# Performance work log

Measured on AMD Instinct MI355X. Metric: run time of the kernel, lower is better.

The kernel has to match this reference:

```python
import jax, jax.numpy as jnp
import numpy as np

NUM_HEADS = 16
D_MODEL = 1024
DEPTH = D_MODEL // NUM_HEADS


def rope_sincos(seq_len, depth):
    # standard RoPE: inv_freq over even dims, sin/cos tiled to full depth
    inv_freq = 1.0 / (10000.0 ** (jnp.arange(0, depth, 2, dtype=jnp.float32) / depth))
    ang = jnp.arange(seq_len, dtype=jnp.float32)[:, None] * inv_freq[None, :]  # [S, depth/2]
    sin = jnp.concatenate([jnp.sin(ang), jnp.sin(ang)], axis=-1)  # [S, depth]
    cos = jnp.concatenate([jnp.cos(ang), jnp.cos(ang)], axis=-1)
    return sin, cos


def apply_rope(x, sin, cos):
    # x: [B,H,S,depth]; rotate-half formulation
    half = x.shape[-1] // 2
    x1, x2 = x[..., :half], x[..., half:]
    rot = jnp.concatenate([-x2, x1], axis=-1)
    return x * cos + rot * sin


def setup_inputs() -> dict:
    key = jax.random.key(0)
    ks = jax.random.split(key, 5)
    s = 1.0 / np.sqrt(D_MODEL)
    return {
        "x": jax.random.normal(ks[0], (2, 2048, D_MODEL), dtype=jnp.float32),
        "wq": jax.random.normal(ks[1], (D_MODEL, D_MODEL), dtype=jnp.float32) * s,
        "bq": jnp.zeros((D_MODEL,), jnp.float32),
        "wk": jax.random.normal(ks[2], (D_MODEL, D_MODEL), dtype=jnp.float32) * s,
        "bk": jnp.zeros((D_MODEL,), jnp.float32),
        "wv": jax.random.normal(ks[3], (D_MODEL, D_MODEL), dtype=jnp.float32) * s,
        "bv": jnp.zeros((D_MODEL,), jnp.float32),
        "wo": jax.random.normal(ks[4], (D_MODEL, D_MODEL), dtype=jnp.float32) * s,
        "bo": jnp.zeros((D_MODEL,), jnp.float32),
    }


def reference(x, wq, bq, wk, bk, wv, bv, wo, bo):
    B, S, _ = x.shape

    def split_heads(t):  # [B,S,D] -> [B,H,S,depth]
        return t.reshape(B, S, NUM_HEADS, DEPTH).transpose(0, 2, 1, 3)

    Q = split_heads(x @ wq + bq)
    K = split_heads(x @ wk + bk)
    V = split_heads(x @ wv + bv)

    sin, cos = rope_sincos(S, DEPTH)  # [S, depth], broadcasts over B,H
    Q = apply_rope(Q, sin, cos)
    K = apply_rope(K, sin, cos)

    scores = jnp.einsum("bhqd,bhkd->bhqk", Q, K) / jnp.sqrt(jnp.float32(DEPTH))
    weights = jax.nn.softmax(scores, axis=-1)
    out = jnp.einsum("bhqk,bhkd->bhqd", weights, V)
    out = out.transpose(0, 2, 1, 3).reshape(B, S, D_MODEL)
    return out @ wo + bo
```

## Files before the change

kernel.cpp:

```cpp
#include <hip/hip_runtime.h>

#define DM 1024
#define SEQ 2048
#define NH 16
#define DH 64
#define BATCH 2

typedef _Float16 half_t;
typedef _Float16 half8 __attribute__((ext_vector_type(8)));
typedef _Float16 half4 __attribute__((ext_vector_type(4)));
typedef __fp16 f16x2 __attribute__((ext_vector_type(2)));
typedef unsigned u32x2 __attribute__((ext_vector_type(2)));
typedef unsigned u32x4 __attribute__((ext_vector_type(4)));
typedef float f32x4 __attribute__((ext_vector_type(4)));

__device__ __forceinline__ f32x4 mfma16(half8 a, half8 b, f32x4 c) {
  return __builtin_amdgcn_mfma_f32_16x16x32_f16(a, b, c, 0, 0, 0);
}
__device__ __forceinline__ f32x4 mfma16k16(half4 a, half4 b, f32x4 c) {
  return __builtin_amdgcn_mfma_f32_16x16x16f16(a, b, c, 0, 0, 0);
}

__device__ __forceinline__ void gl2lds16(const half_t* g, half_t* l) {
  __builtin_amdgcn_global_load_lds((const __attribute__((address_space(1))) void*)g,
                                   (__attribute__((address_space(3))) void*)l, 16, 0, 0);
}


__global__ void cvt_x_kernel(const float* __restrict__ x, half_t* __restrict__ xh) {
  int i = (blockIdx.x * 256 + threadIdx.x) * 4;
  float4 v = *(const float4*)(x + i);
  half4 h = { (half_t)v.x, (half_t)v.y, (half_t)v.z, (half_t)v.w };
  *(half4*)(xh + i) = h;
}

__global__ void wtrans_kernel(const float* __restrict__ w0, const float* __restrict__ w1,
                              const float* __restrict__ w2, const float* __restrict__ w3,
                              half_t* __restrict__ o0, half_t* __restrict__ o1,
                              half_t* __restrict__ o2, half_t* __restrict__ o3) {
  __shared__ float tile[32][33];
  const float* w = (blockIdx.z == 0) ? w0 : (blockIdx.z == 1) ? w1 : (blockIdx.z == 2) ? w2 : w3;
  half_t* o = (blockIdx.z == 0) ? o0 : (blockIdx.z == 1) ? o1 : (blockIdx.z == 2) ? o2 : o3;
  int tx = threadIdx.x, ty0 = threadIdx.y;
  int bx = blockIdx.x * 32, by = blockIdx.y * 32;
#pragma unroll
  for (int i = 0; i < 4; i++) {
    int ty = ty0 + i * 8;
    tile[ty][tx] = w[(size_t)(by + ty) * DM + bx + tx];
  }
  __syncthreads();
#pragma unroll
  for (int i = 0; i < 4; i++) {
    int ty = ty0 + i * 8;
    o[(size_t)(bx + ty) * DM + by + tx] = (half_t)tile[tx][ty];
  }
}

__global__ void ropetab_kernel(float* __restrict__ st, float* __restrict__ ct) {
  int idx = blockIdx.x * 256 + threadIdx.x;
  int s = idx >> 5, i = idx & 31;
  float freq = exp2f(-(float)i * (13.287712379549449f / 32.0f));
  float ang = (float)s * freq;
  st[idx] = sinf(ang);
  ct[idx] = cosf(ang);
}


__global__ __launch_bounds__(256)
void qkv_kernel(const half_t* __restrict__ xh,
                const half_t* __restrict__ wtq, const half_t* __restrict__ wtk,
                const half_t* __restrict__ wtv,
                const float* __restrict__ bq, const float* __restrict__ bk,
                const float* __restrict__ bv,
                const float* __restrict__ st, const float* __restrict__ ctab,
                half_t* __restrict__ Qh, half_t* __restrict__ Kh, half_t* __restrict__ Vt) {
  const int tid = threadIdx.x;
  const int wid = tid >> 6, lane = tid & 63;
  const int l16 = lane & 15, quad = lane >> 4;
  const int m0 = blockIdx.y * 128, n0 = blockIdx.x * 128;
  const int g = blockIdx.z;
  const half_t* wt = (g == 0) ? wtq : (g == 1) ? wtk : wtv;
  const float* bias = (g == 0) ? bq : (g == 1) ? bk : bv;
  __shared__ __align__(16) char smem[32768];
  f32x4 acc[4][4] = {};
  const int wrow = (wid >> 1) * 64, wcol = (wid & 1) * 64;

  const int ar0 = tid >> 2,          ab0 = (tid & 3) ^ ((ar0 >> 1) & 3);
  const int ar1 = (tid + 256) >> 2,  ab1 = (tid & 3) ^ ((ar1 >> 1) & 3);
  const int swz = (l16 >> 1) & 3;

  {
    half_t* As = (half_t*)smem;
    half_t* Bs = (half_t*)(smem + 16384);
    gl2lds16(&xh[(size_t)(m0 + ar0) * DM + ab0 * 8], &As[tid * 8]);
    gl2lds16(&xh[(size_t)(m0 + ar1) * DM + ab1 * 8], &As[(tid + 256) * 8]);
    gl2lds16(&wt[(size_t)(n0 + ar0) * DM + ab0 * 8], &Bs[tid * 8]);
    gl2lds16(&wt[(size_t)(n0 + ar1) * DM + ab1 * 8], &Bs[(tid + 256) * 8]);
  }
  __syncthreads();

  int cur = 0;
  for (int k0 = 0; k0 < DM; k0 += 32) {
    if (k0 + 32 < DM) {
      half_t* Asn = (half_t*)(smem + (cur ^ 1) * 8192);
      half_t* Bsn = (half_t*)(smem + 16384 + (cur ^ 1) * 8192);
      const int kn = k0 + 32;
      gl2lds16(&xh[(size_t)(m0 + ar0) * DM + kn + ab0 * 8], &Asn[tid * 8]);
      gl2lds16(&xh[(size_t)(m0 + ar1) * DM + kn + ab1 * 8], &Asn[(tid + 256) * 8]);
      gl2lds16(&wt[(size_t)(n0 + ar0) * DM + kn + ab0 * 8], &Bsn[tid * 8]);
      gl2lds16(&wt[(size_t)(n0 + ar1) * DM + kn + ab1 * 8], &Bsn[(tid + 256) * 8]);
    }
    const half_t* Asc = (const half_t*)(smem + cur * 8192);
    const half_t* Bsc = (const half_t*)(smem + 16384 + cur * 8192);
    half8 a[4], b[4];
#pragma unroll
    for (int rt = 0; rt < 4; rt++)
      a[rt] = *(const half8*)&Asc[((wrow + rt * 16 + l16) * 4 + (quad ^ swz)) * 8];
#pragma unroll
    for (int ct = 0; ct < 4; ct++)
      b[ct] = *(const half8*)&Bsc[((wcol + ct * 16 + l16) * 4 + (quad ^ swz)) * 8];
#pragma unroll
    for (int rt = 0; rt < 4; rt++)
#pragma unroll
      for (int ct = 0; ct < 4; ct++)
        acc[rt][ct] = mfma16(a[rt], b[ct], acc[rt][ct]);
    __syncthreads();
    cur ^= 1;
  }

  const int h = (n0 + wcol) >> 6;
  const float qscale = 0.125f * 1.44269504089f;
  float bv4[4];
#pragma unroll
  for (int ct = 0; ct < 4; ct++) bv4[ct] = bias[n0 + wcol + ct * 16 + l16];

  if (g == 2) {
    half_t* vt = (half_t*)(smem + wid * 8192);
#pragma unroll
    for (int rt = 0; rt < 4; rt++)
#pragma unroll
      for (int ct = 0; ct < 4; ct++) {
        half4 hv;
#pragma unroll
        for (int r = 0; r < 4; r++) hv[r] = (half_t)(acc[rt][ct][r] + bv4[ct]);
        int row = ct * 16 + l16;
        int colu = rt * 2 + (quad >> 1);
        *(half4*)&vt[row * 64 + ((colu ^ (row & 7)) * 8) + (quad & 1) * 4] = hv;
      }
    const int sb = m0 + wrow;
    const int bb = sb >> 11, s0 = sb & 2047;
    half_t* dstv = Vt + (size_t)(bb * NH + h) * DH * SEQ;
#pragma unroll
    for (int i = 0; i < 8; i++) {
      int d = i * 8 + (lane >> 3), c = lane & 7;
      half8 v = *(const half8*)&vt[d * 64 + ((c ^ (d & 7)) * 8)];
      *(half8*)&dstv[(size_t)d * SEQ + s0 + c * 8] = v;
    }
  } else {
    half_t* dst = (g == 0) ? Qh : Kh;
#pragma unroll
    for (int rt = 0; rt < 4; rt++) {
#pragma unroll
      for (int r = 0; r < 4; r++) {
        int m = m0 + wrow + rt * 16 + quad * 4 + r;
        int bb = m >> 11, s = m & 2047;
        float v0 = acc[rt][0][r] + bv4[0];
        float v1 = acc[rt][1][r] + bv4[1];
        float v2 = acc[rt][2][r] + bv4[2];
        float v3 = acc[rt][3][r] + bv4[3];
        float sn0 = st[s * 32 + l16], cs0 = ctab[s * 32 + l16];
        float sn1 = st[s * 32 + 16 + l16], cs1 = ctab[s * 32 + 16 + l16];
        float o0 = v0 * cs0 - v2 * sn0;
        float o1 = v1 * cs1 - v3 * sn1;
        float o2 = v2 * cs0 + v0 * sn0;
        float o3 = v3 * cs1 + v1 * sn1;
        if (g == 0) { o0 *= qscale; o1 *= qscale; o2 *= qscale; o3 *= qscale; }
        size_t base = ((size_t)(bb * NH + h) * SEQ + s) * DH;
        dst[base + l16]      = (half_t)o0;
        dst[base + 16 + l16] = (half_t)o1;
        dst[base + 32 + l16] = (half_t)o2;
        dst[base + 48 + l16] = (half_t)o3;
      }
    }
  }
}


__global__ __launch_bounds__(512)
void attn_kernel(const half_t* __restrict__ Qh, const half_t* __restrict__ Kh,
                 const half_t* __restrict__ Vt, half_t* __restrict__ AO) {
  const int tid = threadIdx.x;
  const int wid = tid >> 6, lane = tid & 63;
  const int l16 = lane & 15, quad = lane >> 4;
  const int lid = blockIdx.x;
  const int bh = lid & 31, qt = lid >> 5;
  const int bb = bh >> 4, h = bh & 15;
  const int q0 = qt * 256 + wid * 32;
  const half_t* Q = Qh + (size_t)bh * SEQ * DH;
  const half_t* K = Kh + (size_t)bh * SEQ * DH;
  const half_t* V = Vt + (size_t)bh * DH * SEQ;
  __shared__ __align__(16) half_t Ks[2][64 * 64];
  __shared__ __align__(16) half_t Vs[2][64 * 64];

  const int r0 = tid >> 3, c0 = (tid & 7) ^ (r0 & 7);
  const int sw0 = ((quad ^ (l16 & 7)) * 8);
  const int sw1 = (((quad + 4) ^ (l16 & 7)) * 8);

  const half_t* gK0 = &K[(size_t)r0 * DH + c0 * 8];
  const half_t* gV0 = &V[(size_t)r0 * SEQ + c0 * 8];

  half8 aqA[2], aqB[2];
#pragma unroll
  for (int rt = 0; rt < 2; rt++) {
    aqA[rt] = *(const half8*)&Q[(size_t)(q0 + rt * 16 + l16) * DH + quad * 8];
    aqB[rt] = *(const half8*)&Q[(size_t)(q0 + rt * 16 + l16) * DH + 32 + quad * 8];
  }

  f32x4 o[2][4] = {};
  f32x4 vsum[2] = {};
  const f32x4 cinit = {-12.f, -12.f, -12.f, -12.f};

  gl2lds16(gK0, &Ks[0][tid * 8]);
  gl2lds16(gV0, &Vs[0][tid * 8]);
  __syncthreads();

  int cur = 0;
  for (int kb0 = 0; kb0 < SEQ; kb0 += 64) {
    const bool pf = (kb0 + 64 < SEQ);
    u32x4 rk0, rv0;
    if (pf) {
      const int kb = kb0 + 64;
      rk0 = *(const u32x4*)(gK0 + (size_t)kb * DH);
      rv0 = *(const u32x4*)(gV0 + kb);
    }
    const half_t* ksrc = Ks[cur];
    const half_t* vsrc = Vs[cur];

    f32x4 z[2][4];
    __builtin_amdgcn_s_setprio(1);
#pragma unroll
    for (int kt = 0; kt < 4; kt++) {
      const half_t* krow = &ksrc[(kt * 16 + l16) * 64];
      half8 b0 = *(const half8*)&krow[sw0];
      half8 b1 = *(const half8*)&krow[sw1];
#pragma unroll
      for (int rt = 0; rt < 2; rt++) {
        f32x4 zz = cinit;
        zz = mfma16(b0, aqA[rt], zz);
        zz = mfma16(b1, aqB[rt], zz);
        z[rt][kt] = zz;
      }
    }
    __builtin_amdgcn_s_setprio(0);

    half4 pa[2][4];
#pragma unroll
    for (int rt = 0; rt < 2; rt++)
#pragma unroll
      for (int kt = 0; kt < 4; kt++) {
        f32x4 p;
#pragma unroll
        for (int r = 0; r < 4; r++) p[r] = __builtin_amdgcn_exp2f(z[rt][kt][r]);
        vsum[rt] += p;
        f16x2 lo = __builtin_amdgcn_cvt_pkrtz(p[0], p[1]);
        f16x2 hi = __builtin_amdgcn_cvt_pkrtz(p[2], p[3]);
        u32x2 w = { __builtin_bit_cast(unsigned, lo), __builtin_bit_cast(unsigned, hi) };
        pa[rt][kt] = __builtin_bit_cast(half4, w);
      }

    __builtin_amdgcn_s_setprio(1);
#pragma unroll
    for (int dt = 0; dt < 4; dt++) {
      const int row = dt * 16 + l16;
      const half_t* vrow = &vsrc[row * 64 + (quad & 1) * 4];
#pragma unroll
      for (int kt = 0; kt < 4; kt++) {
        half4 bv = *(const half4*)&vrow[((kt * 2 + (quad >> 1)) ^ (l16 & 7)) * 8];
#pragma unroll
        for (int rt = 0; rt < 2; rt++)
          o[rt][dt] = mfma16k16(pa[rt][kt], bv, o[rt][dt]);
      }
    }
    __builtin_amdgcn_s_setprio(0);

    if (pf) {
      const int nxt = cur ^ 1;
      *(u32x4*)&Ks[nxt][tid * 8] = rk0;
      *(u32x4*)&Vs[nxt][tid * 8] = rv0;
    }
    __syncthreads();
    cur ^= 1;
  }

  float linv[2][4];
#pragma unroll
  for (int rt = 0; rt < 2; rt++) {
    float s = (vsum[rt][0] + vsum[rt][1]) + (vsum[rt][2] + vsum[rt][3]);
    s += __shfl_xor(s, 16);
    s += __shfl_xor(s, 32);
#pragma unroll
    for (int r = 0; r < 4; r++) linv[rt][r] = 1.f / __shfl(s, quad * 4 + r);
  }
#pragma unroll
  for (int rt = 0; rt < 2; rt++)
#pragma unroll
    for (int dt = 0; dt < 4; dt++)
#pragma unroll
      for (int r = 0; r < 4; r++) {
        int srow = q0 + rt * 16 + quad * 4 + r;
        AO[((size_t)bb * SEQ + srow) * DM + h * DH + dt * 16 + l16] =
            (half_t)(o[rt][dt][r] * linv[rt][r]);
      }
}


__global__ __launch_bounds__(256)
void out_kernel(const half_t* __restrict__ AO, const half_t* __restrict__ wto,
                const float* __restrict__ bo, float* __restrict__ out) {
  const int tid = threadIdx.x;
  const int wid = tid >> 6, lane = tid & 63;
  const int l16 = lane & 15, quad = lane >> 4;
  const int m0 = blockIdx.y * 128, n0 = blockIdx.x * 64;
  __shared__ __align__(16) char smem[24576];
  f32x4 acc[4][2] = {};
  const int wrow = (wid >> 1) * 64, wcol = (wid & 1) * 32;

  const int ar0 = tid >> 2,         ab0 = (tid & 3) ^ ((ar0 >> 1) & 3);
  const int ar1 = (tid + 256) >> 2, ab1 = (tid & 3) ^ ((ar1 >> 1) & 3);
  const int swz = (l16 >> 1) & 3;

  {
    half_t* As = (half_t*)smem;
    half_t* Bs = (half_t*)(smem + 16384);
    gl2lds16(&AO[(size_t)(m0 + ar0) * DM + ab0 * 8], &As[tid * 8]);
    gl2lds16(&AO[(size_t)(m0 + ar1) * DM + ab1 * 8], &As[(tid + 256) * 8]);
    gl2lds16(&wto[(size_t)(n0 + ar0) * DM + ab0 * 8], &Bs[tid * 8]);
  }
  __syncthreads();

  int cur = 0;
  for (int k0 = 0; k0 < DM; k0 += 32) {
    if (k0 + 32 < DM) {
      half_t* Asn = (half_t*)(smem + (cur ^ 1) * 8192);
      half_t* Bsn = (half_t*)(smem + 16384 + (cur ^ 1) * 4096);
      const int kn = k0 + 32;
      gl2lds16(&AO[(size_t)(m0 + ar0) * DM + kn + ab0 * 8], &Asn[tid * 8]);
      gl2lds16(&AO[(size_t)(m0 + ar1) * DM + kn + ab1 * 8], &Asn[(tid + 256) * 8]);
      gl2lds16(&wto[(size_t)(n0 + ar0) * DM + kn + ab0 * 8], &Bsn[tid * 8]);
    }
    const half_t* Asc = (const half_t*)(smem + cur * 8192);
    const half_t* Bsc = (const half_t*)(smem + 16384 + cur * 4096);
    half8 a[4], b[2];
#pragma unroll
    for (int rt = 0; rt < 4; rt++)
      a[rt] = *(const half8*)&Asc[((wrow + rt * 16 + l16) * 4 + (quad ^ swz)) * 8];
#pragma unroll
    for (int ct = 0; ct < 2; ct++)
      b[ct] = *(const half8*)&Bsc[((wcol + ct * 16 + l16) * 4 + (quad ^ swz)) * 8];
#pragma unroll
    for (int rt = 0; rt < 4; rt++)
#pragma unroll
      for (int ct = 0; ct < 2; ct++)
        acc[rt][ct] = mfma16(a[rt], b[ct], acc[rt][ct]);
    __syncthreads();
    cur ^= 1;
  }
  float bv2[2];
#pragma unroll
  for (int ct = 0; ct < 2; ct++) bv2[ct] = bo[n0 + wcol + ct * 16 + l16];
#pragma unroll
  for (int rt = 0; rt < 4; rt++)
#pragma unroll
    for (int r = 0; r < 4; r++) {
      int m = m0 + wrow + rt * 16 + quad * 4 + r;
#pragma unroll
      for (int ct = 0; ct < 2; ct++)
        out[(size_t)m * DM + n0 + wcol + ct * 16 + l16] = acc[rt][ct][r] + bv2[ct];
    }
}


extern "C" void kernel_launch(void* const* d_in, const int* in_sizes, int n_in,
                              void* d_out, int out_size, void* d_ws, size_t ws_size,
                              hipStream_t stream) {
  (void)in_sizes; (void)n_in; (void)out_size; (void)ws_size;
  const float* x  = (const float*)d_in[0];
  const float* wq = (const float*)d_in[1];
  const float* bq = (const float*)d_in[2];
  const float* wk = (const float*)d_in[3];
  const float* bk = (const float*)d_in[4];
  const float* wv = (const float*)d_in[5];
  const float* bv = (const float*)d_in[6];
  const float* wo = (const float*)d_in[7];
  const float* bo = (const float*)d_in[8];
  char* ws = (char*)d_ws;
  const size_t MB = 1u << 20;
  half_t* xh  = (half_t*)(ws + 0);
  half_t* AO  = (half_t*)(ws + 0);
  half_t* wtq = (half_t*)(ws + 8 * MB);
  half_t* wtk = (half_t*)(ws + 10 * MB);
  half_t* wtv = (half_t*)(ws + 12 * MB);
  half_t* wto = (half_t*)(ws + 14 * MB);
  float*  st  = (float*)(ws + 16 * MB);
  float*  ctb = (float*)(ws + 16 * MB + 256 * 1024);
  half_t* Qh  = (half_t*)(ws + 17 * MB);
  half_t* Kh  = (half_t*)(ws + 25 * MB);
  half_t* Vt  = (half_t*)(ws + 33 * MB);
  float* out = (float*)d_out;

  cvt_x_kernel<<<4096, 256, 0, stream>>>(x, xh);
  wtrans_kernel<<<dim3(32, 32, 4), dim3(32, 8), 0, stream>>>(wq, wk, wv, wo, wtq, wtk, wtv, wto);
  ropetab_kernel<<<256, 256, 0, stream>>>(st, ctb);
  qkv_kernel<<<dim3(8, 32, 3), 256, 0, stream>>>(xh, wtq, wtk, wtv, bq, bk, bv, st, ctb, Qh, Kh, Vt);
  attn_kernel<<<256, 512, 0, stream>>>(Qh, Kh, Vt, AO);
  out_kernel<<<dim3(16, 32), 256, 0, stream>>>(AO, wto, bo, out);
}
```

Before: 194.1 us.

## Fuse prep kernels into one launch and halve attention block size

Merges the x conversion, weight transpose and RoPE table kernels into a single prep launch that dispatches on block index, removing two kernel launches. The attention kernel now runs 4 waves per block covering 128 queries instead of 8 waves covering 256, with a 512-block grid. Each thread now loads two K/V chunks per tile to fill the shared buffers. More blocks improve load spread across CUs, but each K/V tile is re-read from global memory by twice as many blocks.

```diff
diff --git a/kernel.cpp b/kernel.cpp
--- a/kernel.cpp
+++ b/kernel.cpp
@@ -27,42 +27,49 @@
 }
 
 
-__global__ void cvt_x_kernel(const float* __restrict__ x, half_t* __restrict__ xh) {
-  int i = (blockIdx.x * 256 + threadIdx.x) * 4;
-  float4 v = *(const float4*)(x + i);
-  half4 h = { (half_t)v.x, (half_t)v.y, (half_t)v.z, (half_t)v.w };
-  *(half4*)(xh + i) = h;
-}
-
-__global__ void wtrans_kernel(const float* __restrict__ w0, const float* __restrict__ w1,
-                              const float* __restrict__ w2, const float* __restrict__ w3,
-                              half_t* __restrict__ o0, half_t* __restrict__ o1,
-                              half_t* __restrict__ o2, half_t* __restrict__ o3) {
+__global__ __launch_bounds__(256)
+void prep_kernel(const float* __restrict__ x,
+                 const float* __restrict__ w0, const float* __restrict__ w1,
+                 const float* __restrict__ w2, const float* __restrict__ w3,
+                 half_t* __restrict__ xh,
+                 half_t* __restrict__ o0, half_t* __restrict__ o1,
+                 half_t* __restrict__ o2, half_t* __restrict__ o3,
+                 float* __restrict__ st, float* __restrict__ ct) {
   __shared__ float tile[32][33];
-  const float* w = (blockIdx.z == 0) ? w0 : (blockIdx.z == 1) ? w1 : (blockIdx.z == 2) ? w2 : w3;
-  half_t* o = (blockIdx.z == 0) ? o0 : (blockIdx.z == 1) ? o1 : (blockIdx.z == 2) ? o2 : o3;
-  int tx = threadIdx.x, ty0 = threadIdx.y;
-  int bx = blockIdx.x * 32, by = blockIdx.y * 32;
-#pragma unroll
-  for (int i = 0; i < 4; i++) {
-    int ty = ty0 + i * 8;
-    tile[ty][tx] = w[(size_t)(by + ty) * DM + bx + tx];
-  }
-  __syncthreads();
-#pragma unroll
-  for (int i = 0; i < 4; i++) {
-    int ty = ty0 + i * 8;
-    o[(size_t)(bx + ty) * DM + by + tx] = (half_t)tile[tx][ty];
-  }
-}
-
-__global__ void ropetab_kernel(float* __restrict__ st, float* __restrict__ ct) {
-  int idx = blockIdx.x * 256 + threadIdx.x;
-  int s = idx >> 5, i = idx & 31;
-  float freq = exp2f(-(float)i * (13.287712379549449f / 32.0f));
-  float ang = (float)s * freq;
-  st[idx] = sinf(ang);
-  ct[idx] = cosf(ang);
+  const int lid = blockIdx.x;
+  const int tid = threadIdx.x;
+  if (lid < 4096) {
+    int i = (lid * 256 + tid) * 4;
+    float4 v = *(const float4*)(x + i);
+    half4 h = { (half_t)v.x, (half_t)v.y, (half_t)v.z, (half_t)v.w };
+    *(half4*)(xh + i) = h;
+  } else if (lid < 8192) {
+    int l = lid - 4096;
+    int z = l >> 10;
+    int by = (l >> 5) & 31, bx = l & 31;
+    const float* w = (z == 0) ? w0 : (z == 1) ? w1 : (z == 2) ? w2 : w3;
+    half_t* o = (z == 0) ? o0 : (z == 1) ? o1 : (z == 2) ? o2 : o3;
+    int tx = tid & 31, ty0 = tid >> 5;
+    int bxx = bx * 32, byy = by * 32;
+#pragma unroll
+    for (int i = 0; i < 4; i++) {
+      int ty = ty0 + i * 8;
+      tile[ty][tx] = w[(size_t)(byy + ty) * DM + bxx + tx];
+    }
+    __syncthreads();
+#pragma unroll
+    for (int i = 0; i < 4; i++) {
+      int ty = ty0 + i * 8;
+      o[(size_t)(bxx + ty) * DM + byy + tx] = (half_t)tile[tx][ty];
+    }
+  } else {
+    int idx = (lid - 8192) * 256 + tid;
+    int s = idx >> 5, i = idx & 31;
+    float freq = exp2f(-(float)i * (13.287712379549449f / 32.0f));
+    float ang = (float)s * freq;
+    st[idx] = sinf(ang);
+    ct[idx] = cosf(ang);
+  }
 }
 
 
@@ -186,7 +193,7 @@
 }
 
 
-__global__ __launch_bounds__(512)
+__global__ __launch_bounds__(256)
 void attn_kernel(const half_t* __restrict__ Qh, const half_t* __restrict__ Kh,
                  const half_t* __restrict__ Vt, half_t* __restrict__ AO) {
   const int tid = threadIdx.x;
@@ -195,19 +202,22 @@
   const int lid = blockIdx.x;
   const int bh = lid & 31, qt = lid >> 5;
   const int bb = bh >> 4, h = bh & 15;
-  const int q0 = qt * 256 + wid * 32;
+  const int q0 = qt * 128 + wid * 32;
   const half_t* Q = Qh + (size_t)bh * SEQ * DH;
   const half_t* K = Kh + (size_t)bh * SEQ * DH;
   const half_t* V = Vt + (size_t)bh * DH * SEQ;
   __shared__ __align__(16) half_t Ks[2][64 * 64];
   __shared__ __align__(16) half_t Vs[2][64 * 64];
 
-  const int r0 = tid >> 3, c0 = (tid & 7) ^ (r0 & 7);
+  const int r0 = tid >> 3,         c0 = (tid & 7) ^ (r0 & 7);
+  const int r1 = (tid + 256) >> 3, c1 = (tid & 7) ^ (r1 & 7);
   const int sw0 = ((quad ^ (l16 & 7)) * 8);
   const int sw1 = (((quad + 4) ^ (l16 & 7)) * 8);
 
   const half_t* gK0 = &K[(size_t)r0 * DH + c0 * 8];
+  const half_t* gK1 = &K[(size_t)r1 * DH + c1 * 8];
   const half_t* gV0 = &V[(size_t)r0 * SEQ + c0 * 8];
+  const half_t* gV1 = &V[(size_t)r1 * SEQ + c1 * 8];
 
   half8 aqA[2], aqB[2];
 #pragma unroll
@@ -221,17 +231,21 @@
   const f32x4 cinit = {-12.f, -12.f, -12.f, -12.f};
 
   gl2lds16(gK0, &Ks[0][tid * 8]);
+  gl2lds16(gK1, &Ks[0][(tid + 256) * 8]);
   gl2lds16(gV0, &Vs[0][tid * 8]);
+  gl2lds16(gV1, &Vs[0][(tid + 256) * 8]);
   __syncthreads();
 
   int cur = 0;
   for (int kb0 = 0; kb0 < SEQ; kb0 += 64) {
     const bool pf = (kb0 + 64 < SEQ);
-    u32x4 rk0, rv0;
+    u32x4 rk0, rk1, rv0, rv1;
     if (pf) {
       const int kb = kb0 + 64;
       rk0 = *(const u32x4*)(gK0 + (size_t)kb * DH);
+      rk1 = *(const u32x4*)(gK1 + (size_t)kb * DH);
       rv0 = *(const u32x4*)(gV0 + kb);
+      rv1 = *(const u32x4*)(gV1 + kb);
     }
     const half_t* ksrc = Ks[cur];
     const half_t* vsrc = Vs[cur];
@@ -286,7 +300,9 @@
     if (pf) {
       const int nxt = cur ^ 1;
       *(u32x4*)&Ks[nxt][tid * 8] = rk0;
+      *(u32x4*)&Ks[nxt][(tid + 256) * 8] = rk1;
       *(u32x4*)&Vs[nxt][tid * 8] = rv0;
+      *(u32x4*)&Vs[nxt][(tid + 256) * 8] = rv1;
     }
     __syncthreads();
     cur ^= 1;
@@ -408,10 +424,8 @@
   half_t* Vt  = (half_t*)(ws + 33 * MB);
   float* out = (float*)d_out;
 
-  cvt_x_kernel<<<4096, 256, 0, stream>>>(x, xh);
-  wtrans_kernel<<<dim3(32, 32, 4), dim3(32, 8), 0, stream>>>(wq, wk, wv, wo, wtq, wtk, wtv, wto);
-  ropetab_kernel<<<256, 256, 0, stream>>>(st, ctb);
+  prep_kernel<<<8448, 256, 0, stream>>>(x, wq, wk, wv, wo, xh, wtq, wtk, wtv, wto, st, ctb);
   qkv_kernel<<<dim3(8, 32, 3), 256, 0, stream>>>(xh, wtq, wtk, wtv, bq, bk, bv, st, ctb, Qh, Kh, Vt);
-  attn_kernel<<<256, 512, 0, stream>>>(Qh, Kh, Vt, AO);
+  attn_kernel<<<512, 256, 0, stream>>>(Qh, Kh, Vt, AO);
   out_kernel<<<dim3(16, 32), 256, 0, stream>>>(AO, wto, bo, out);
 }
```

Result: no change. 194.0 us (-0.1%).
